# Performance work log

Hardware: AMD Instinct MI355X
Metric: run time of the kernel (lower is better)

The kernel has to match this reference:

```python
import jax, jax.numpy as jnp
import numpy as np

N, E = 4096, 65536
H = 200
KS = (3072, 1536, 768)  # ceil(0.75*4096), ceil(0.5*3072), ceil(0.5*1536)


def _gcn(A, x, W, b):
    # GCNConv with improved=True: A_hat = A + 2I, sym-normalized
    n = A.shape[0]
    Ah = A + 2.0 * jnp.eye(n, dtype=A.dtype)
    dinv = jax.lax.rsqrt(Ah.sum(axis=1))
    An = dinv[:, None] * Ah * dinv[None, :]
    return An @ (x @ W) + b


def _augment(A):
    # GraphUNet.augment_adj: remove self loops, add self loops (w=1), spspmm(A,A), remove self loops
    n = A.shape[0]
    eye = jnp.eye(n, dtype=A.dtype)
    Ap = A * (1.0 - eye) + eye
    A2 = Ap @ Ap  # dense form of spspmm (two-hop adjacency with weights)
    return A2 * (1.0 - eye)


def _pool(A, x, pw, k):
    # TopKPooling: score = tanh(x.w/||w||), keep top-k, scale kept x by score
    score = jnp.tanh((x @ pw) / jnp.linalg.norm(pw))
    val, perm = jax.lax.top_k(score, k)
    return x[perm] * val[:, None], A[perm][:, perm], perm


def _unet(x, adj, w0, b0, w1, b1, w2, b2, w3, b3, p1, p2, p3,
          u0w, u0b, u1w, u1b, u2w, u2b):
    down = [(w1, b1), (w2, b2), (w3, b3)]
    pws = [p1, p2, p3]
    up = [(u0w, u0b), (u1w, u1b), (u2w, u2b)]
    x = jax.nn.relu(_gcn(adj, x, w0, b0))
    xs, As, perms = [x], [adj], []
    A = adj
    for i in range(3):
        A = _augment(A)
        x, A, perm = _pool(A, x, pws[i], KS[i])
        x = jax.nn.relu(_gcn(A, x, *down[i]))
        if i < 2:
            xs.append(x)
            As.append(A)
        perms.append(perm)
    for i in range(3):
        j = 2 - i
        upf = jnp.zeros_like(xs[j]).at[perms[j]].set(x)
        x = xs[j] + upf  # sum_res=True
        x = _gcn(As[j], x, *up[i])
        if i < 2:
            x = jax.nn.relu(x)
    return jax.nn.log_softmax(x, axis=1)


def setup_inputs() -> dict:
    key = jax.random.key(0)
    ks = jax.random.split(key, 16)
    x = jax.random.normal(ks[0], (N, 3), dtype=jnp.float32)
    src = jax.random.randint(ks[1], (E,), 0, N)
    dst = jax.random.randint(ks[2], (E,), 0, N)
    A = jnp.zeros((N, N), jnp.float32).at[src, dst].set(1.0)
    A = jnp.maximum(A, A.T) * (1.0 - jnp.eye(N, dtype=jnp.float32))
    g = lambda k, s: jax.random.normal(k, s, jnp.float32) * 0.1
    z = lambda n: jnp.zeros((n,), jnp.float32)
    return dict(
        x=x, adj=A,
        w0=g(ks[3], (3, H)), b0=z(H),
        w1=g(ks[4], (H, H)), b1=z(H),
        w2=g(ks[5], (H, H)), b2=z(H),
        w3=g(ks[6], (H, H)), b3=z(H),
        p1=g(ks[7], (H,)), p2=g(ks[8], (H,)), p3=g(ks[9], (H,)),
        u0w=g(ks[10], (H, H)), u0b=z(H),
        u1w=g(ks[11], (H, H)), u1b=z(H),
        u2w=g(ks[12], (H, 2)), u2b=z(2),
    )


def reference(x, adj, w0, b0, w1, b1, w2, b2, w3, b3, p1, p2, p3,
              u0w, u0b, u1w, u1b, u2w, u2b):
    return _unet(x, adj, w0, b0, w1, b1, w2, b2, w3, b3, p1, p2, p3,
                 u0w, u0b, u1w, u1b, u2w, u2b)
```

## Files before the change

### kernel.cpp

```cpp
#include <hip/hip_runtime.h>

typedef unsigned short u16;
typedef unsigned int u32;
typedef unsigned long long u64;
typedef signed char s8;
typedef __attribute__((ext_vector_type(8))) short bfrag8;
typedef __attribute__((ext_vector_type(4))) float f32x4;
typedef __attribute__((ext_vector_type(4))) int i32x4;
typedef __attribute__((address_space(1))) const void gconst_void;
typedef __attribute__((address_space(3))) void lds_void_t;

__device__ __forceinline__ float bf2f(u16 u) {
  return __uint_as_float(((u32)u) << 16);
}
__device__ __forceinline__ u16 f2bf(float f) {
  u32 u = __float_as_uint(f);
  u32 r = (u + 0x7FFFu + ((u >> 16) & 1u)) >> 16;
  return (u16)r;
}
__device__ __forceinline__ void split3(float v, u16& hi, u16& mi, u16& lo) {
  hi = f2bf(v); float r1 = v - bf2f(hi);
  mi = f2bf(r1); float r2 = r1 - bf2f(mi);
  lo = f2bf(r2);
}
__device__ __forceinline__ float ld1(const void* p, int isbf, long idx) {
  return isbf ? bf2f(((const u16*)p)[idx]) : ((const float*)p)[idx];
}
__device__ __forceinline__ void ld4(const void* p, int isbf, long base, long gc, long bound, float v[4]) {
  if (gc + 3 < bound && ((base & 3) == 0)) {
    if (isbf) {
      const ushort4 u = *(const ushort4*)((const u16*)p + base);
      v[0] = bf2f(u.x); v[1] = bf2f(u.y); v[2] = bf2f(u.z); v[3] = bf2f(u.w);
    } else {
      const float4 f = *(const float4*)((const float*)p + base);
      v[0] = f.x; v[1] = f.y; v[2] = f.z; v[3] = f.w;
    }
  } else {
    #pragma unroll
    for (int d = 0; d < 4; ++d) v[d] = (gc + d < bound) ? ld1(p, isbf, base + d) : 0.f;
  }
}

__global__ void detect_k(const u32* __restrict__ a, long nw, int* __restrict__ flag) {
  long stride = (long)gridDim.x * 256;
  int f = 0;
  for (long j = (long)blockIdx.x * 256 + threadIdx.x; j < nw; j += stride) {
    u32 w = a[j];
    if (w == 0x00003F80u || w == 0x3F803F80u) f = 1;
  }
  if (__any(f)) {
    if ((threadIdx.x & 63) == 0) atomicOr(flag, 1);
  }
}

__device__ __forceinline__ int get_bf(int abf, const int* dtf) {
  return (abf >= 0) ? abf : *dtf;
}

__device__ __forceinline__ void stageB16(const void* g, void* lds) {
#if __has_builtin(__builtin_amdgcn_global_load_lds)
  __builtin_amdgcn_global_load_lds((gconst_void*)g, (lds_void_t*)lds, 16, 0, 0);
#else
  int lane = threadIdx.x & 63;
  *(int4*)((char*)lds + lane * 16) = *(const int4*)g;
#endif
}

__global__ __launch_bounds__(256) void syrk_tri_i8_parts(
    const s8* __restrict__ Ag, int ldk, int Ksplit, int ntri,
    int* __restrict__ parts)
{
  __shared__ s8 At[128 * 64];
  __shared__ s8 Bt[128 * 64];
  const int t = blockIdx.x;
  int ti = (int)((sqrtf((float)(8 * t + 1)) - 1.0f) * 0.5f);
  while ((ti + 1) * (ti + 2) / 2 <= t) ++ti;
  while (ti * (ti + 1) / 2 > t) --ti;
  const int tj = t - ti * (ti + 1) / 2;

  const int tid = threadIdx.x;
  const int wave = tid >> 6, lane = tid & 63;
  const int wr = wave >> 1, wc = wave & 1;
  const long rowA0 = (long)ti * 128;
  const long rowB0 = (long)tj * 128;
  const int kbeg = blockIdx.y * Ksplit;
  const int kend = kbeg + Ksplit;

  i32x4 acc[4][4];
  #pragma unroll
  for (int i = 0; i < 4; ++i)
    #pragma unroll
    for (int j = 0; j < 4; ++j) acc[i][j] = (i32x4)0;

  const int srow = lane >> 2;
  const int scol = (lane & 3) * 16;
  const int m = lane & 15, q = lane >> 4;

  for (int k0 = kbeg; k0 < kend; k0 += 64) {
    #pragma unroll
    for (int tt = 0; tt < 2; ++tt) {
      const int r = wave * 32 + tt * 16;
      stageB16(Ag + (rowA0 + r + srow) * (long)ldk + k0 + scol, At + r * 64);
      stageB16(Ag + (rowB0 + r + srow) * (long)ldk + k0 + scol, Bt + r * 64);
    }
    __syncthreads();

    i32x4 af[4], bf[4];
    #pragma unroll
    for (int mt = 0; mt < 4; ++mt)
      af[mt] = *(const i32x4*)(At + (wr * 64 + mt * 16 + m) * 64 + q * 16);
    #pragma unroll
    for (int nt = 0; nt < 4; ++nt)
      bf[nt] = *(const i32x4*)(Bt + (wc * 64 + nt * 16 + m) * 64 + q * 16);
    #pragma unroll
    for (int mt = 0; mt < 4; ++mt)
      #pragma unroll
      for (int nt = 0; nt < 4; ++nt)
        acc[mt][nt] = __builtin_amdgcn_mfma_i32_16x16x64_i8(af[mt], bf[nt], acc[mt][nt], 0, 0, 0);
    __syncthreads();
  }

  int* P = parts + ((long)blockIdx.y * ntri + t) * 16384;
  #pragma unroll
  for (int mt = 0; mt < 4; ++mt) {
    #pragma unroll
    for (int nt = 0; nt < 4; ++nt) {
      const int r0 = wr * 64 + mt * 16 + q * 4;
      const int c = wc * 64 + nt * 16 + m;
      #pragma unroll
      for (int r = 0; r < 4; ++r)
        P[(r0 + r) * 128 + c] = acc[mt][nt][r];
    }
  }
}

__global__ __launch_bounds__(256) void reduce_tri_i8_k(
    const int* __restrict__ parts, int ntri, int n, int nz,
    u16* __restrict__ Ah, u16* __restrict__ Al)
{
  __shared__ float T[128 * 33];
  const int t = blockIdx.x >> 2;
  const int slab = blockIdx.x & 3;
  int ti = (int)((sqrtf((float)(8 * t + 1)) - 1.0f) * 0.5f);
  while ((ti + 1) * (ti + 2) / 2 <= t) ++ti;
  while (ti * (ti + 1) / 2 > t) --ti;
  const int tj = t - ti * (ti + 1) / 2;
  const long rowA0 = (long)ti * 128;
  const long rowB0 = (long)tj * 128;
  const int r0 = slab * 32;
  const int tid = threadIdx.x;
  const long tstride = (long)ntri * 16384;

  #pragma unroll
  for (int it = 0; it < 16; ++it) {
    const int idx = it * 256 + tid;
    const int lr = idx >> 7;
    const int lc = idx & 127;
    long base = (long)t * 16384 + (r0 + lr) * 128 + lc;
    int v = 0;
    for (int z = 0; z < nz; ++z) v += parts[(long)z * tstride + base];
    const long gr = rowA0 + r0 + lr;
    const long gc = rowB0 + lc;
    if (gr == gc) v = 0;
    const float fv = (float)v;
    const u16 h = f2bf(fv);
    const long o = gr * n + gc;
    Ah[o] = h;
    if (Al) Al[o] = f2bf(fv - bf2f(h));
    T[lc * 33 + lr] = fv;
  }
  if (ti == tj) return;
  __syncthreads();
  #pragma unroll
  for (int it = 0; it < 16; ++it) {
    const int idx = it * 256 + tid;
    const int mr = idx >> 5;
    const int mc = idx & 31;
    const float fv = T[mr * 33 + mc];
    const u16 h = f2bf(fv);
    const long o = (rowB0 + mr) * n + rowA0 + r0 + mc;
    Ah[o] = h;
    if (Al) Al[o] = f2bf(fv - bf2f(h));
  }
}

__global__ void rowsum_planes_k(const u16* __restrict__ Ah, const u16* __restrict__ Al,
                                int n, double* __restrict__ rs) {
  __shared__ double red[256];
  const int row = blockIdx.x, tid = threadIdx.x;
  const uint4* A4 = (const uint4*)(Ah + (long)row * n);
  const uint4* L4 = Al ? (const uint4*)(Al + (long)row * n) : nullptr;
  const int n8 = n >> 3;
  double s = 0.0;
  for (int j = tid; j < n8; j += 256) {
    uint4 u = A4[j];
    float v = bf2f((u16)(u.x & 0xFFFFu)) + bf2f((u16)(u.x >> 16))
            + bf2f((u16)(u.y & 0xFFFFu)) + bf2f((u16)(u.y >> 16))
            + bf2f((u16)(u.z & 0xFFFFu)) + bf2f((u16)(u.z >> 16))
            + bf2f((u16)(u.w & 0xFFFFu)) + bf2f((u16)(u.w >> 16));
    if (L4) {
      uint4 l = L4[j];
      v += bf2f((u16)(l.x & 0xFFFFu)) + bf2f((u16)(l.x >> 16))
         + bf2f((u16)(l.y & 0xFFFFu)) + bf2f((u16)(l.y >> 16))
         + bf2f((u16)(l.z & 0xFFFFu)) + bf2f((u16)(l.z >> 16))
         + bf2f((u16)(l.w & 0xFFFFu)) + bf2f((u16)(l.w >> 16));
    }
    s += (double)v;
  }
  red[tid] = s; __syncthreads();
  for (int st = 128; st > 0; st >>= 1) {
    if (tid < st) red[tid] += red[tid + st];
    __syncthreads();
  }
  if (tid == 0) rs[row] = red[0];
}

__global__ __launch_bounds__(256) void syrk_tri2_parts(
    const u16* __restrict__ Ah, const u16* __restrict__ Al, int ldk,
    float* __restrict__ parts, int n, int per)
{
  __shared__ u16 Ath[128 * 32];
  __shared__ u16 Bth[128 * 32];
  __shared__ u16 Atl[128 * 32];
  __shared__ u16 Btl[128 * 32];
  const int t = blockIdx.x;
  int ti = (int)((sqrtf((float)(8 * t + 1)) - 1.0f) * 0.5f);
  while ((ti + 1) * (ti + 2) / 2 <= t) ++ti;
  while (ti * (ti + 1) / 2 > t) --ti;
  const int tj = t - ti * (ti + 1) / 2;

  const int tid = threadIdx.x;
  const int wave = tid >> 6, lane = tid & 63;
  const int wr = wave >> 1, wc = wave & 1;
  const long rowA0 = (long)ti * 128;
  const long rowB0 = (long)tj * 128;
  const int kbeg = blockIdx.y * per;
  const int kend = kbeg + per;

  f32x4 acc[4][4];
  #pragma unroll
  for (int i = 0; i < 4; ++i)
    #pragma unroll
    for (int j = 0; j < 4; ++j) acc[i][j] = (f32x4)0.f;

  const int srow = lane >> 2;
  const int scol = (lane & 3) * 8;
  const int m = lane & 15, q = lane >> 4;

  for (int k0 = kbeg; k0 < kend; k0 += 32) {
    #pragma unroll
    for (int tt = 0; tt < 2; ++tt) {
      const int r = wave * 32 + tt * 16;
      stageB16(Ah + (rowA0 + r + srow) * (long)ldk + k0 + scol, Ath + r * 32);
      stageB16(Ah + (rowB0 + r + srow) * (long)ldk + k0 + scol, Bth + r * 32);
      stageB16(Al + (rowA0 + r + srow) * (long)ldk + k0 + scol, Atl + r * 32);
      stageB16(Al + (rowB0 + r + srow) * (long)ldk + k0 + scol, Btl + r * 32);
    }
    __syncthreads();

    bfrag8 afh[4], afl[4], bfh[4], bfl[4];
    #pragma unroll
    for (int mt = 0; mt < 4; ++mt) {
      afh[mt] = *(const bfrag8*)(Ath + (wr * 64 + mt * 16 + m) * 32 + q * 8);
      afl[mt] = *(const bfrag8*)(Atl + (wr * 64 + mt * 16 + m) * 32 + q * 8);
    }
    #pragma unroll
    for (int nt = 0; nt < 4; ++nt) {
      bfh[nt] = *(const bfrag8*)(Bth + (wc * 64 + nt * 16 + m) * 32 + q * 8);
      bfl[nt] = *(const bfrag8*)(Btl + (wc * 64 + nt * 16 + m) * 32 + q * 8);
    }
    #pragma unroll
    for (int mt = 0; mt < 4; ++mt)
      #pragma unroll
      for (int nt = 0; nt < 4; ++nt) {
        acc[mt][nt] = __builtin_amdgcn_mfma_f32_16x16x32_bf16(afh[mt], bfh[nt], acc[mt][nt], 0, 0, 0);
        acc[mt][nt] = __builtin_amdgcn_mfma_f32_16x16x32_bf16(afh[mt], bfl[nt], acc[mt][nt], 0, 0, 0);
        acc[mt][nt] = __builtin_amdgcn_mfma_f32_16x16x32_bf16(afl[mt], bfh[nt], acc[mt][nt], 0, 0, 0);
        acc[mt][nt] = __builtin_amdgcn_mfma_f32_16x16x32_bf16(afl[mt], bfl[nt], acc[mt][nt], 0, 0, 0);
      }
    __syncthreads();
  }

  float* P = parts + (long)blockIdx.y * n * n;
  #pragma unroll
  for (int mt = 0; mt < 4; ++mt) {
    #pragma unroll
    for (int nt = 0; nt < 4; ++nt) {
      const long gr0 = rowA0 + wr * 64 + mt * 16 + q * 4;
      const long gc = rowB0 + wc * 64 + nt * 16 + m;
      #pragma unroll
      for (int r = 0; r < 4; ++r)
        P[(gr0 + r) * n + gc] = acc[mt][nt][r];
    }
  }
}

__global__ void reduce_tri_mirror_k(const float* __restrict__ parts,
                                    u16* __restrict__ Ah, u16* __restrict__ Al,
                                    double* __restrict__ rsum, int n, int nz) {
  __shared__ double red[256];
  const int tid = threadIdx.x;
  long idx = (long)blockIdx.x * 256 + tid;
  long nn = (long)n * n;
  long r = idx / n, c = idx - r * n;
  double myv = 0.0;
  if (idx < nn) {
    if (r == c) {
      Ah[idx] = 0; Al[idx] = 0;
    } else if (r > c) {
      float s = 0.f;
      for (int z = 0; z < nz; ++z) s += parts[(long)z * nn + r * n + c];
      long mi = c * n + r;
      u16 h = f2bf(s);
      u16 l = f2bf(s - bf2f(h));
      Ah[idx] = h; Al[idx] = l;
      Ah[mi] = h;  Al[mi] = l;
      myv = (double)s;
      atomicAdd(&rsum[c], (double)s);
    }
  }
  red[tid] = myv;
  __syncthreads();
  for (int st = 128; st > 0; st >>= 1) {
    if (tid < st) red[tid] += red[tid + st];
    __syncthreads();
  }
  if (tid == 0 && idx < nn) atomicAdd(&rsum[r], red[0]);
}

__global__ void bg_i8_k(const void* __restrict__ src, int srcbf, int nsrc,
                        const int* __restrict__ perm, int kRows,
                        s8* __restrict__ Ag, const int* __restrict__ dtf,
                        const float* __restrict__ xsrc, const float* __restrict__ score,
                        float* __restrict__ xdst, unsigned nbB) {
  if (blockIdx.x < nbB) {
    long tot = (long)kRows * nsrc;
    long idx = (long)blockIdx.x * 256 + threadIdx.x;
    if (idx >= tot) return;
    int r = (int)(idx / nsrc);
    int c = (int)(idx - (long)r * nsrc);
    int p = perm[r];
    float v = ld1(src, get_bf(srcbf, dtf), (long)p * nsrc + c);
    if (c == p) v += 1.f;
    Ag[idx] = (s8)(int)v;
  } else {
    long tot = (long)kRows * 200;
    long idx = (long)(blockIdx.x - nbB) * 256 + threadIdx.x;
    if (idx >= tot) return;
    int r = (int)(idx / 200);
    int c = (int)(idx - (long)r * 200);
    int p = perm[r];
    xdst[idx] = xsrc[(long)p * 200 + c] * score[p];
  }
}

__global__ void bg_sp_k(const u16* __restrict__ srcH, const u16* __restrict__ srcL,
                        int nsrc, const int* __restrict__ perm, int kRows,
                        u16* __restrict__ Agh, u16* __restrict__ Agl,
                        const float* __restrict__ xsrc, const float* __restrict__ score,
                        float* __restrict__ xdst, unsigned nbB) {
  if (blockIdx.x < nbB) {
    long tot = (long)kRows * nsrc;
    long idx = (long)blockIdx.x * 256 + threadIdx.x;
    if (idx >= tot) return;
    int r = (int)(idx / nsrc);
    int c = (int)(idx - (long)r * nsrc);
    int p = perm[r];
    long si = (long)p * nsrc + c;
    float v = bf2f(srcH[si]) + bf2f(srcL[si]);
    if (c == p) v += 1.f;
    u16 h = f2bf(v);
    Agh[idx] = h;
    Agl[idx] = f2bf(v - bf2f(h));
  } else {
    long tot = (long)kRows * 200;
    long idx = (long)(blockIdx.x - nbB) * 256 + threadIdx.x;
    if (idx >= tot) return;
    int r = (int)(idx / 200);
    int c = (int)(idx - (long)r * 200);
    int p = perm[r];
    xdst[idx] = xsrc[(long)p * 200 + c] * score[p];
  }
}

template<int NT, int HASAL>
__global__ __launch_bounds__(512) void agg_mfma8(
    const u16* __restrict__ Ah, const u16* __restrict__ Al,
    const u16* __restrict__ ZT, float* __restrict__ parts,
    int K, int per_steps)
{
  constexpr int CT0 = (NT + 1) / 2;
  constexpr int NZT = 3 * NT;
  constexpr int NSTG = (HASAL ? 16 : 8) + NZT;
  __shared__ u16 At[2][8 * 512];
  __shared__ u16 Alt[(HASAL ? 2 : 1)][8 * 512];
  __shared__ u16 Zt[2][NZT * 512];

  const int tid = threadIdx.x;
  const int wave = tid >> 6, lane = tid & 63;
  const int rg = wave & 3;
  const int cg = wave >> 2;
  const int ct_base = cg ? CT0 : 0;
  const int nct = cg ? (NT - CT0) : CT0;
  const long row0 = (long)blockIdx.x * 128;
  const int chunk = blockIdx.y;
  const int kbeg = chunk * per_steps * 32;
  const int nsteps = (min(K, kbeg + per_steps * 32) - kbeg) / 32;
  const int m = lane & 15, q = lane >> 4;
  const int srow = lane >> 2, scol = (lane & 3) * 8;

  auto stage = [&](int buf, int k0) {
    u16* Atb = At[buf];
    u16* Ztb = Zt[buf];
    u16* Altb = Alt[HASAL ? buf : 0];
    for (int s = wave; s < NSTG; s += 8) {
      if (s < 8) {
        stageB16(Ah + (row0 + s * 16 + srow) * (long)K + k0 + scol, Atb + s * 512);
      } else if (HASAL && s < 16) {
        stageB16(Al + (row0 + (s - 8) * 16 + srow) * (long)K + k0 + scol, Altb + (s - 8) * 512);
      } else {
        const int z = s - (HASAL ? 16 : 8);
        stageB16(ZT + ((long)(z * 16 + srow)) * K + k0 + scol, Ztb + z * 512);
      }
    }
  };

  f32x4 acc[2][CT0];
  #pragma unroll
  for (int rt = 0; rt < 2; ++rt)
    #pragma unroll
    for (int ct = 0; ct < CT0; ++ct) acc[rt][ct] = (f32x4)0.f;

  stage(0, kbeg);
  __syncthreads();
  int cur = 0;
  for (int t = 0; t < nsteps; ++t) {
    if (t + 1 < nsteps) stage(cur ^ 1, kbeg + (t + 1) * 32);

    const u16* Atb = At[cur];
    const u16* Ztb = Zt[cur];
    bfrag8 af0 = *(const bfrag8*)(Atb + (rg * 2) * 512 + m * 32 + q * 8);
    bfrag8 af1 = *(const bfrag8*)(Atb + (rg * 2 + 1) * 512 + m * 32 + q * 8);
    bfrag8 al0, al1;
    if (HASAL) {
      const u16* Altb = Alt[cur];
      al0 = *(const bfrag8*)(Altb + (rg * 2) * 512 + m * 32 + q * 8);
      al1 = *(const bfrag8*)(Altb + (rg * 2 + 1) * 512 + m * 32 + q * 8);
    }
    #pragma unroll
    for (int ct = 0; ct < CT0; ++ct) {
      if (ct < nct) {
        const int c = ct_base + ct;
        bfrag8 b0 = *(const bfrag8*)(Ztb + (0 * NT + c) * 512 + m * 32 + q * 8);
        bfrag8 b1 = *(const bfrag8*)(Ztb + (1 * NT + c) * 512 + m * 32 + q * 8);
        bfrag8 b2 = *(const bfrag8*)(Ztb + (2 * NT + c) * 512 + m * 32 + q * 8);
        acc[0][ct] = __builtin_amdgcn_mfma_f32_16x16x32_bf16(af0, b0, acc[0][ct], 0, 0, 0);
        acc[0][ct] = __builtin_amdgcn_mfma_f32_16x16x32_bf16(af0, b1, acc[0][ct], 0, 0, 0);
        acc[0][ct] = __builtin_amdgcn_mfma_f32_16x16x32_bf16(af0, b2, acc[0][ct], 0, 0, 0);
        acc[1][ct] = __builtin_amdgcn_mfma_f32_16x16x32_bf16(af1, b0, acc[1][ct], 0, 0, 0);
        acc[1][ct] = __builtin_amdgcn_mfma_f32_16x16x32_bf16(af1, b1, acc[1][ct], 0, 0, 0);
        acc[1][ct] = __builtin_amdgcn_mfma_f32_16x16x32_bf16(af1, b2, acc[1][ct], 0, 0, 0);
        if (HASAL) {
          acc[0][ct] = __builtin_amdgcn_mfma_f32_16x16x32_bf16(al0, b0, acc[0][ct], 0, 0, 0);
          acc[0][ct] = __builtin_amdgcn_mfma_f32_16x16x32_bf16(al0, b1, acc[0][ct], 0, 0, 0);
          acc[1][ct] = __builtin_amdgcn_mfma_f32_16x16x32_bf16(al1, b0, acc[1][ct], 0, 0, 0);
          acc[1][ct] = __builtin_amdgcn_mfma_f32_16x16x32_bf16(al1, b1, acc[1][ct], 0, 0, 0);
        }
      }
    }
    if (t + 1 < nsteps) __syncthreads();
    cur ^= 1;
  }

  float* P = parts + (long)chunk * gridDim.x * 128 * (NT * 16);
  #pragma unroll
  for (int rt = 0; rt < 2; ++rt) {
    #pragma unroll
    for (int ct = 0; ct < CT0; ++ct) {
      if (ct < nct) {
        const long grow0 = row0 + rg * 32 + rt * 16 + q * 4;
        const long gcol = (ct_base + ct) * 16 + m;
        #pragma unroll
        for (int r = 0; r < 4; ++r)
          P[(grow0 + r) * (NT * 16) + gcol] = acc[rt][ct][r];
      }
    }
  }
}

__global__ __launch_bounds__(256) void reduce_epi_k(
    const float* __restrict__ parts, const float* __restrict__ Zs,
    const double* __restrict__ rs, const float* __restrict__ b,
    float* __restrict__ out, int n, int nz, int relu,
    const float* __restrict__ pw, float* __restrict__ score)
{
  __shared__ float vrow[200];
  const int i = blockIdx.x, tid = threadIdx.x;
  float dv = (float)(1.0 / sqrt(rs[i] + 2.0));
  if (tid < 200) {
    long base = (long)i * 208 + tid;
    float s = 0.f;
    for (int c = 0; c < nz; ++c) s += parts[(long)c * n * 208 + base];
    float v = dv * (s + 2.f * Zs[(long)i * 200 + tid]) + b[tid];
    if (relu) v = fmaxf(v, 0.f);
    out[(long)i * 200 + tid] = v;
    if (score) vrow[tid] = v;
  }
  if (!score) return;
  __syncthreads();
  if (tid < 64) {
    double ps = 0.0;
    for (int j = tid; j < 200; j += 64) { double w = pw[j]; ps += w * w; }
    for (int off = 32; off > 0; off >>= 1) ps += __shfl_down(ps, off);
    double nrm = sqrt(__shfl(ps, 0));
    double s = 0.0;
    for (int j = tid; j < 200; j += 64) s += (double)vrow[j] * (double)pw[j];
    for (int off = 32; off > 0; off >>= 1) s += __shfl_down(s, off);
    if (tid == 0) score[i] = (float)tanh(s / nrm);
  }
}

__global__ void a_from_adj_rs_k(const void* __restrict__ adj, const int* __restrict__ dtf,
                                int n, u16* __restrict__ Ah, double* __restrict__ rs) {
  __shared__ double red[256];
  int bf = *dtf;
  const int row = blockIdx.x, tid = threadIdx.x;
  const long base = (long)row * n;
  double s = 0.0;
  for (int j = tid; j < n; j += 256) {
    float v = ld1(adj, bf, base + j);
    Ah[base + j] = bf ? ((const u16*)adj)[base + j] : f2bf(v);
    s += (double)v;
  }
  red[tid] = s; __syncthreads();
  for (int st = 128; st > 0; st >>= 1) {
    if (tid < st) red[tid] += red[tid + st];
    __syncthreads();
  }
  if (tid == 0) rs[row] = red[0];
}

__global__ __launch_bounds__(256) void gemm64_f64(
    const void* __restrict__ Ap, long lda, int abf,
    const void* __restrict__ Bp, long ldb, int bbf,
    float* __restrict__ C, long ldc, int M, int N, int K,
    const double* __restrict__ rsum, u16* __restrict__ ZT, const int* __restrict__ dtf)
{
  const int abf_ = get_bf(abf, dtf);
  const int bbf_ = get_bf(bbf, dtf);
  __shared__ float As[16][64];
  __shared__ float Bs[16][64];
  const int tid = threadIdx.x;
  const int tr = tid >> 4, tc = tid & 15;
  const long row0 = (long)blockIdx.y * 64;
  const long col0 = (long)blockIdx.x * 64;
  double acc[4][4];
  #pragma unroll
  for (int i = 0; i < 4; ++i)
    #pragma unroll
    for (int j = 0; j < 4; ++j) acc[i][j] = 0.0;

  const int am = tid >> 2;
  const int ak = (tid & 3) * 4;
  const int bk = tid >> 4;
  const int bn = (tid & 15) * 4;

  for (int k0 = 0; k0 < K; k0 += 16) {
    float va[4] = {0.f, 0.f, 0.f, 0.f};
    {
      long gm = row0 + am; long gk = k0 + ak;
      if (gm < M && gk < K) ld4(Ap, abf_, gm * lda + gk, gk, K, va);
    }
    As[ak + 0][am] = va[0]; As[ak + 1][am] = va[1];
    As[ak + 2][am] = va[2]; As[ak + 3][am] = va[3];

    float vb[4] = {0.f, 0.f, 0.f, 0.f};
    {
      long gk = k0 + bk; long gn = col0 + bn;
      if (gk < K && gn < N) ld4(Bp, bbf_, gk * ldb + gn, gn, N, vb);
    }
    Bs[bk][bn + 0] = vb[0]; Bs[bk][bn + 1] = vb[1];
    Bs[bk][bn + 2] = vb[2]; Bs[bk][bn + 3] = vb[3];

    __syncthreads();
    #pragma unroll
    for (int kk = 0; kk < 16; ++kk) {
      float a[4], b[4];
      #pragma unroll
      for (int i = 0; i < 4; ++i) a[i] = As[kk][tr * 4 + i];
      #pragma unroll
      for (int j = 0; j < 4; ++j) b[j] = Bs[kk][tc * 4 + j];
      #pragma unroll
      for (int i = 0; i < 4; ++i)
        #pragma unroll
        for (int j = 0; j < 4; ++j)
          acc[i][j] += (double)a[i] * (double)b[j];
    }
    __syncthreads();
  }
  #pragma unroll
  for (int i = 0; i < 4; ++i) {
    long gm = row0 + tr * 4 + i;
    if (gm >= M) continue;
    float sc = rsum ? (float)(1.0 / sqrt(rsum[gm] + 2.0)) : 1.f;
    #pragma unroll
    for (int j = 0; j < 4; ++j) {
      long gn = col0 + tc * 4 + j;
      if (gn < N) {
        float v0 = (float)acc[i][j];
        float v = v0 * sc;
        C[gm * ldc + gn] = v;
        if (ZT) {
          u16 hi, mi, lo; split3(v, hi, mi, lo);
          ZT[((long)0 * 208 + gn) * M + gm] = hi;
          ZT[((long)1 * 208 + gn) * M + gm] = mi;
          ZT[((long)2 * 208 + gn) * M + gm] = lo;
        }
      }
    }
  }
}

struct UpBatch {
  const void* src[19];
  float* dst[19];
  int n[19];
};

__global__ void upcast_batch_k(UpBatch ub, const int* __restrict__ dtf) {
  int bf = *dtf;
  int a = blockIdx.y;
  int i = blockIdx.x * 256 + threadIdx.x;
  if (i < ub.n[a]) ub.dst[a][i] = ld1(ub.src[a], bf, i);
}

template<int V>
__global__ __launch_bounds__(1024) void topk_fast(const float* __restrict__ score,
                                                  int n, int np2, int k,
                                                  int* __restrict__ perm,
                                                  int* __restrict__ inv) {
  __shared__ u64 keys[4096];
  const int tid = threadIdx.x;
  const int REGMAX = 32 * V;
  for (int i = tid; i < n; i += 1024) inv[i] = -1;
  u64 kreg[V];
  #pragma unroll
  for (int r = 0; r < V; ++r) {
    int i = tid * V + r;
    u64 key = 0ULL;
    if (i < n) {
      u32 b = __float_as_uint(score[i]);
      u32 u = (b & 0x80000000u) ? ~b : (b | 0x80000000u);
      key = ((u64)u << 32) | (u32)(~(u32)i);
    }
    kreg[r] = key;
  }

  for (int size = 2; size <= np2; size <<= 1) {
    int stride = size >> 1;
    if (stride > REGMAX) {
      #pragma unroll
      for (int r = 0; r < V; ++r) keys[tid * V + r] = kreg[r];
      __syncthreads();
      for (; stride > REGMAX; stride >>= 1) {
        for (int i = tid; i < np2; i += 1024) {
          int j = i ^ stride;
          if (j > i) {
            u64 a = keys[i], b = keys[j];
            bool up = ((i & size) == 0);
            if (up ? (a > b) : (a < b)) { keys[i] = b; keys[j] = a; }
          }
        }
        __syncthreads();
      }
      #pragma unroll
      for (int r = 0; r < V; ++r) kreg[r] = keys[tid * V + r];
    }
    for (; stride >= 1; stride >>= 1) {
      if (stride >= V) {
        int lm = stride / V;
        #pragma unroll
        for (int r = 0; r < V; ++r) {
          u64 mine = kreg[r];
          u64 other = (u64)__shfl_xor((long long)mine, lm);
          int i = tid * V + r;
          bool up = ((i & size) == 0);
          bool lower = ((i & stride) == 0);
          u64 mn = mine < other ? mine : other;
          u64 mx = mine < other ? other : mine;
          kreg[r] = (lower == up) ? mn : mx;
        }
      } else {
        #pragma unroll
        for (int r = 0; r < V; ++r) {
          int pr = r ^ stride;
          if (pr > r) {
            int i = tid * V + r;
            bool up = ((i & size) == 0);
            u64 a = kreg[r], b = kreg[pr];
            if (up ? (a > b) : (a < b)) { kreg[r] = b; kreg[pr] = a; }
          }
        }
      }
    }
  }
  #pragma unroll
  for (int r = 0; r < V; ++r) {
    int i = tid * V + r;
    int rank = np2 - 1 - i;
    if (rank < k) {
      int idx = (int)(~(u32)(kreg[r] & 0xFFFFFFFFull));
      perm[rank] = idx;
      inv[idx] = rank;
    }
  }
}

__global__ void upadd_k(const float* __restrict__ xs, const float* __restrict__ xpool,
                        const int* __restrict__ inv, float* __restrict__ dst, long nh, int h) {
  long idx = (long)blockIdx.x * 256 + threadIdx.x;
  if (idx >= nh) return;
  int i = (int)(idx / h);
  int c = (int)(idx - (long)i * h);
  float v = xs[idx];
  int r = inv[i];
  if (r >= 0) v += xpool[(long)r * h + c];
  dst[idx] = v;
}

__global__ void matvec2_final_k(const void* __restrict__ A, int abf, int n,
                                const float* __restrict__ Zs, const double* __restrict__ rs0,
                                const float* __restrict__ b2, float* __restrict__ out,
                                const int* __restrict__ dtf) {
  const int bf = get_bf(abf, dtf);
  int row = blockIdx.x, tid = threadIdx.x;
  const long base = (long)row * n;
  double s0 = 0.0, s1 = 0.0;
  for (int j = tid; j < n; j += 256) {
    double a = (double)ld1(A, bf, base + j);
    s0 += a * (double)Zs[2 * j];
    s1 += a * (double)Zs[2 * j + 1];
  }
  __shared__ double r0[256], r1[256];
  r0[tid] = s0; r1[tid] = s1; __syncthreads();
  for (int st = 128; st > 0; st >>= 1) {
    if (tid < st) { r0[tid] += r0[tid + st]; r1[tid] += r1[tid + st]; }
    __syncthreads();
  }
  if (tid == 0) {
    double y0 = (double)((float)r0[0]);
    double y1 = (double)((float)r1[0]);
    double di = (double)((float)(1.0 / sqrt(rs0[row] + 2.0)));
    double t0 = di * (y0 + 2.0 * (double)Zs[2 * row]) + (double)b2[0];
    double t1 = di * (y1 + 2.0 * (double)Zs[2 * row + 1]) + (double)b2[1];
    double mx = fmax(t0, t1);
    double l = mx + log(exp(t0 - mx) + exp(t1 - mx));
    out[2 * row] = (float)(t0 - l);
    out[2 * row + 1] = (float)(t1 - l);
  }
}

extern "C" void kernel_launch(void* const* d_in, const int* in_sizes, int n_in,
                              void* d_out, int out_size, void* d_ws, size_t ws_size,
                              hipStream_t stream) {
  const int N0 = 4096, H = 200;
  const int K1 = 3072, K2 = 1536, K3 = 768;

  const void* in_x = d_in[0];
  const void* adj  = d_in[1];
  const void* w0 = d_in[2];  const void* b0 = d_in[3];
  const void* w1 = d_in[4];  const void* b1 = d_in[5];
  const void* w2 = d_in[6];  const void* b2 = d_in[7];
  const void* w3 = d_in[8];  const void* b3 = d_in[9];
  const void* p1 = d_in[10]; const void* p2 = d_in[11];
  const void* p3 = d_in[12];
  const void* u0w = d_in[13]; const void* u0b = d_in[14];
  const void* u1w = d_in[15]; const void* u1b = d_in[16];
  const void* u2w = d_in[17]; const void* u2b = d_in[18];

  char* wp = (char*)d_ws;
  auto alloc = [&](size_t bytes) -> void* {
    void* p = (void*)wp;
    wp += (bytes + 255) & ~(size_t)255;
    return p;
  };
  size_t partsBytes = (size_t)300 * 4 * 16384 * 4 + 1024;
  float* parts = (float*)alloc(partsBytes);
  s8*    Agb  = (s8*)alloc((size_t)K1 * N0);
  u16* Ag3h = (u16*)alloc((size_t)K3 * K2 * 2);
  u16* Ag3l = (u16*)alloc((size_t)K3 * K2 * 2);
  u16* Ah0 = (u16*)alloc((size_t)N0 * N0 * 2);
  u16* Ah1 = (u16*)alloc((size_t)K1 * K1 * 2);
  u16* Ah2 = (u16*)alloc((size_t)K2 * K2 * 2);
  u16* Al2 = (u16*)alloc((size_t)K2 * K2 * 2);
  u16* Ah3 = (u16*)alloc((size_t)K3 * K3 * 2);
  u16* Al3 = (u16*)alloc((size_t)K3 * K3 * 2);
  u16* ZT  = (u16*)alloc((size_t)3 * 208 * N0 * 2);
  float* xs0  = (float*)alloc((size_t)N0 * H * 4);
  float* xs1  = (float*)alloc((size_t)K1 * H * 4);
  float* xs2  = (float*)alloc((size_t)K2 * H * 4);
  float* xcur = (float*)alloc((size_t)N0 * H * 4);
  float* xtmp = (float*)alloc((size_t)N0 * H * 4);
  float* Zbuf = (float*)alloc((size_t)N0 * H * 4);
  float* Xinf = (float*)alloc((size_t)N0 * 3 * 4);
  double* rs0 = (double*)alloc((size_t)N0 * 8);
  double* rs1 = (double*)alloc((size_t)K1 * 8);
  double* rs2 = (double*)alloc((size_t)K2 * 8);
  double* rs3 = (double*)alloc((size_t)K3 * 8);
  int* dtflag = (int*)alloc(256);
  float* scores = (float*)alloc((size_t)N0 * 4);
  int* perm1 = (int*)alloc((size_t)K1 * 4);
  int* perm2 = (int*)alloc((size_t)K2 * 4);
  int* perm3 = (int*)alloc((size_t)K3 * 4);
  int* inv1 = (int*)alloc((size_t)N0 * 4);
  int* inv2 = (int*)alloc((size_t)K1 * 4);
  int* inv3 = (int*)alloc((size_t)K2 * 4);
  float* w0f = (float*)alloc(3 * H * 4);  float* b0f = (float*)alloc(H * 4);
  float* w1f = (float*)alloc(H * H * 4);  float* b1f = (float*)alloc(H * 4);
  float* w2f = (float*)alloc(H * H * 4);  float* b2f = (float*)alloc(H * 4);
  float* w3f = (float*)alloc(H * H * 4);  float* b3f = (float*)alloc(H * 4);
  float* p1f = (float*)alloc(H * 4);
  float* p2f = (float*)alloc(H * 4);
  float* p3f = (float*)alloc(H * 4);
  float* u0wf = (float*)alloc(H * H * 4); float* u0bf = (float*)alloc(H * 4);
  float* u1wf = (float*)alloc(H * H * 4); float* u1bf = (float*)alloc(H * 4);
  float* u2wf = (float*)alloc(H * 2 * 4); float* u2bf = (float*)alloc(2 * 4);
  (void)in_sizes; (void)n_in; (void)out_size; (void)ws_size;

  hipMemsetAsync(rs1, 0, (size_t)(K1 + K2 + K3) * 8 + 256, stream);
  detect_k<<<dim3(4096), dim3(256), 0, stream>>>((const u32*)adj, (long)N0 * N0 / 2, dtflag);

  {
    UpBatch ub;
    const void* srcs[19] = {in_x, w0, b0, w1, b1, w2, b2, w3, b3, p1, p2, p3,
                            u0w, u0b, u1w, u1b, u2w, u2b, u2b};
    float* dsts[19] = {Xinf, w0f, b0f, w1f, b1f, w2f, b2f, w3f, b3f, p1f, p2f, p3f,
                       u0wf, u0bf, u1wf, u1bf, u2wf, u2bf, u2bf};
    int ns[19] = {N0 * 3, 3 * H, H, H * H, H, H * H, H, H * H, H, H, H, H,
                  H * H, H, H * H, H, H * 2, 2, 2};
    for (int i = 0; i < 19; ++i) { ub.src[i] = srcs[i]; ub.dst[i] = dsts[i]; ub.n[i] = ns[i]; }
    upcast_batch_k<<<dim3((N0 * 3 + 255) / 256, 19), dim3(256), 0, stream>>>(ub, dtflag);
  }

  a_from_adj_rs_k<<<dim3(N0), dim3(256), 0, stream>>>(adj, dtflag, N0, Ah0, rs0);

  auto gemm64 = [&](const void* A, long lda, int abf, const void* B, long ldb, int bbf,
                    float* C, long ldc, int M, int Nn, int K, const double* rsum, u16* zt) {
    dim3 g((Nn + 63) / 64, (M + 63) / 64);
    gemm64_f64<<<g, dim3(256), 0, stream>>>(A, lda, abf, B, ldb, bbf, C, ldc, M, Nn, K,
                                            rsum, zt, dtflag);
  };

  auto gcn = [&](const u16* Ah, const u16* Al, int n, int chunks, const double* rs,
                 const float* Xin_, int din, const float* W, const float* bb,
                 float* out, const float* pwf, float* scoreOut) {
    gemm64(Xin_, din, 0, W, H, 0, Zbuf, H, n, H, din, rs, ZT);
    if (Al)
      agg_mfma8<13, 1><<<dim3(n / 128, chunks), dim3(512), 0, stream>>>(
          Ah, Al, ZT, parts, n, (n / 32) / chunks);
    else
      agg_mfma8<13, 0><<<dim3(n / 128, chunks), dim3(512), 0, stream>>>(
          Ah, nullptr, ZT, parts, n, (n / 32) / chunks);
    reduce_epi_k<<<dim3(n), dim3(256), 0, stream>>>(
        parts, Zbuf, rs, bb, out, n, chunks, 1, pwf, scoreOut);
  };

  gcn(Ah0, nullptr, N0, 8, rs0, Xinf, 3, w0f, b0f, xs0, p1f, scores);

  topk_fast<4><<<dim3(1), dim3(1024), 0, stream>>>(scores, N0, 4096, K1, perm1, inv1);
  {
    unsigned nbB = (unsigned)(((long)K1 * N0 + 255) / 256);
    unsigned nbG = (unsigned)(((long)K1 * 200 + 255) / 256);
    bg_i8_k<<<dim3(nbB + nbG), dim3(256), 0, stream>>>(
        adj, -1, N0, perm1, K1, Agb, dtflag, xs0, scores, xcur, nbB);
    int nt = K1 / 128;
    int ntri = nt * (nt + 1) / 2;
    syrk_tri_i8_parts<<<dim3(ntri, 4), dim3(256), 0, stream>>>(
        Agb, N0, N0 / 4, ntri, (int*)parts);
    reduce_tri_i8_k<<<dim3(ntri * 4), dim3(256), 0, stream>>>(
        (const int*)parts, ntri, K1, 4, Ah1, nullptr);
    rowsum_planes_k<<<dim3(K1), dim3(256), 0, stream>>>(Ah1, nullptr, K1, rs1);
  }
  gcn(Ah1, nullptr, K1, 12, rs1, xcur, H, w1f, b1f, xs1, p2f, scores);

  topk_fast<4><<<dim3(1), dim3(1024), 0, stream>>>(scores, K1, 4096, K2, perm2, inv2);
  {
    unsigned nbB = (unsigned)(((long)K2 * K1 + 255) / 256);
    unsigned nbG = (unsigned)(((long)K2 * 200 + 255) / 256);
    bg_i8_k<<<dim3(nbB + nbG), dim3(256), 0, stream>>>(
        Ah1, 1, K1, perm2, K2, Agb, dtflag, xs1, scores, xcur, nbB);
    int nt = K2 / 128;
    int ntri = nt * (nt + 1) / 2;
    syrk_tri_i8_parts<<<dim3(ntri, 8), dim3(256), 0, stream>>>(
        Agb, K1, K1 / 8, ntri, (int*)parts);
    reduce_tri_i8_k<<<dim3(ntri * 4), dim3(256), 0, stream>>>(
        (const int*)parts, ntri, K2, 8, Ah2, Al2);
    rowsum_planes_k<<<dim3(K2), dim3(256), 0, stream>>>(Ah2, Al2, K2, rs2);
  }
  gcn(Ah2, Al2, K2, 24, rs2, xcur, H, w2f, b2f, xs2, p3f, scores);

  topk_fast<2><<<dim3(1), dim3(1024), 0, stream>>>(scores, K2, 2048, K3, perm3, inv3);
  {
    unsigned nbB = (unsigned)(((long)K3 * K2 + 255) / 256);
    unsigned nbG = (unsigned)(((long)K3 * 200 + 255) / 256);
    bg_sp_k<<<dim3(nbB + nbG), dim3(256), 0, stream>>>(
        Ah2, Al2, K2, perm3, K3, Ag3h, Ag3l, xs2, scores, xcur, nbB);
    int nt = K3 / 128;
    syrk_tri2_parts<<<dim3(nt * (nt + 1) / 2, 8), dim3(256), 0, stream>>>(
        Ag3h, Ag3l, K2, parts, K3, K2 / 8);
    long nn = (long)K3 * K3;
    reduce_tri_mirror_k<<<dim3((unsigned)(nn / 256)), dim3(256), 0, stream>>>(
        parts, Ah3, Al3, rs3, K3, 8);
  }
  gcn(Ah3, Al3, K3, 24, rs3, xcur, H, w3f, b3f, xcur, nullptr, nullptr);

  upadd_k<<<dim3((unsigned)(((long)K2 * H + 255) / 256)), dim3(256), 0, stream>>>(
      xs2, xcur, inv3, xtmp, (long)K2 * H, H);
  gcn(Ah2, Al2, K2, 24, rs2, xtmp, H, u0wf, u0bf, xcur, nullptr, nullptr);

  upadd_k<<<dim3((unsigned)(((long)K1 * H + 255) / 256)), dim3(256), 0, stream>>>(
      xs1, xcur, inv2, xtmp, (long)K1 * H, H);
  gcn(Ah1, nullptr, K1, 12, rs1, xtmp, H, u1wf, u1bf, xcur, nullptr, nullptr);

  upadd_k<<<dim3((unsigned)(((long)N0 * H + 255) / 256)), dim3(256), 0, stream>>>(
      xs0, xcur, inv1, xtmp, (long)N0 * H, H);
  gemm64(xtmp, H, 0, u2wf, 2, 0, Zbuf, 2, N0, 2, H, rs0, nullptr);
  matvec2_final_k<<<dim3(N0), dim3(256), 0, stream>>>(
      adj, -1, N0, Zbuf, rs0, u2bf, (float*)d_out, dtflag);
}
```

Before: 879.6 us.

## Replace single-block bitonic top-k with multi-block rank counting; double-buffer int8 SYRK

After: 848.6 us. 1.04x faster.

```diff
diff --git a/kernel.cpp b/kernel.cpp
--- a/kernel.cpp
+++ b/kernel.cpp
@@ -70,8 +70,8 @@
     const s8* __restrict__ Ag, int ldk, int Ksplit, int ntri,
     int* __restrict__ parts)
 {
-  __shared__ s8 At[128 * 64];
-  __shared__ s8 Bt[128 * 64];
+  __shared__ s8 At[2][128 * 64];
+  __shared__ s8 Bt[2][128 * 64];
   const int t = blockIdx.x;
   int ti = (int)((sqrtf((float)(8 * t + 1)) - 1.0f) * 0.5f);
   while ((ti + 1) * (ti + 2) / 2 <= t) ++ti;
@@ -84,7 +84,7 @@
   const long rowA0 = (long)ti * 128;
   const long rowB0 = (long)tj * 128;
   const int kbeg = blockIdx.y * Ksplit;
-  const int kend = kbeg + Ksplit;
+  const int nsteps = Ksplit / 64;
 
   i32x4 acc[4][4];
   #pragma unroll
@@ -96,28 +96,35 @@
   const int scol = (lane & 3) * 16;
   const int m = lane & 15, q = lane >> 4;
 
-  for (int k0 = kbeg; k0 < kend; k0 += 64) {
+  auto stage = [&](int buf, int k0) {
     #pragma unroll
     for (int tt = 0; tt < 2; ++tt) {
       const int r = wave * 32 + tt * 16;
-      stageB16(Ag + (rowA0 + r + srow) * (long)ldk + k0 + scol, At + r * 64);
-      stageB16(Ag + (rowB0 + r + srow) * (long)ldk + k0 + scol, Bt + r * 64);
-    }
-    __syncthreads();
+      stageB16(Ag + (rowA0 + r + srow) * (long)ldk + k0 + scol, At[buf] + r * 64);
+      stageB16(Ag + (rowB0 + r + srow) * (long)ldk + k0 + scol, Bt[buf] + r * 64);
+    }
+  };
+
+  stage(0, kbeg);
+  __syncthreads();
+  int cur = 0;
+  for (int st = 0; st < nsteps; ++st) {
+    if (st + 1 < nsteps) stage(cur ^ 1, kbeg + (st + 1) * 64);
 
     i32x4 af[4], bf[4];
     #pragma unroll
     for (int mt = 0; mt < 4; ++mt)
-      af[mt] = *(const i32x4*)(At + (wr * 64 + mt * 16 + m) * 64 + q * 16);
+      af[mt] = *(const i32x4*)(At[cur] + (wr * 64 + mt * 16 + m) * 64 + q * 16);
     #pragma unroll
     for (int nt = 0; nt < 4; ++nt)
-      bf[nt] = *(const i32x4*)(Bt + (wc * 64 + nt * 16 + m) * 64 + q * 16);
+      bf[nt] = *(const i32x4*)(Bt[cur] + (wc * 64 + nt * 16 + m) * 64 + q * 16);
     #pragma unroll
     for (int mt = 0; mt < 4; ++mt)
       #pragma unroll
       for (int nt = 0; nt < 4; ++nt)
         acc[mt][nt] = __builtin_amdgcn_mfma_i32_16x16x64_i8(af[mt], bf[nt], acc[mt][nt], 0, 0, 0);
-    __syncthreads();
+    if (st + 1 < nsteps) __syncthreads();
+    cur ^= 1;
   }
 
   int* P = parts + ((long)blockIdx.y * ntri + t) * 16384;
@@ -634,86 +641,57 @@
   if (i < ub.n[a]) ub.dst[a][i] = ld1(ub.src[a], bf, i);
 }
 
-template<int V>
-__global__ __launch_bounds__(1024) void topk_fast(const float* __restrict__ score,
-                                                  int n, int np2, int k,
-                                                  int* __restrict__ perm,
-                                                  int* __restrict__ inv) {
-  __shared__ u64 keys[4096];
+__global__ __launch_bounds__(256) void rank_part_k(
+    const float* __restrict__ score, int n, int ns, int* __restrict__ prank)
+{
+  __shared__ u64 sk[256];
   const int tid = threadIdx.x;
-  const int REGMAX = 32 * V;
-  for (int i = tid; i < n; i += 1024) inv[i] = -1;
-  u64 kreg[V];
-  #pragma unroll
-  for (int r = 0; r < V; ++r) {
-    int i = tid * V + r;
+  const int s = blockIdx.x;
+  const int slice = n / ns;
+  const int jb = s * slice;
+  for (int j = tid; j < slice; j += 256) {
+    int gj = jb + j;
+    u32 b = __float_as_uint(score[gj]);
+    u32 u = (b & 0x80000000u) ? ~b : (b | 0x80000000u);
+    sk[j] = ((u64)u << 32) | (u32)(~(u32)gj);
+  }
+  __syncthreads();
+  const int i0 = tid * 16;
+  if (i0 >= n) return;
+  u64 myk[16];
+  int cnt[16];
+  #pragma unroll
+  for (int e = 0; e < 16; ++e) {
+    int i = i0 + e;
     u64 key = 0ULL;
     if (i < n) {
       u32 b = __float_as_uint(score[i]);
       u32 u = (b & 0x80000000u) ? ~b : (b | 0x80000000u);
       key = ((u64)u << 32) | (u32)(~(u32)i);
     }
-    kreg[r] = key;
-  }
-
-  for (int size = 2; size <= np2; size <<= 1) {
-    int stride = size >> 1;
-    if (stride > REGMAX) {
-      #pragma unroll
-      for (int r = 0; r < V; ++r) keys[tid * V + r] = kreg[r];
-      __syncthreads();
-      for (; stride > REGMAX; stride >>= 1) {
-        for (int i = tid; i < np2; i += 1024) {
-          int j = i ^ stride;
-          if (j > i) {
-            u64 a = keys[i], b = keys[j];
-            bool up = ((i & size) == 0);
-            if (up ? (a > b) : (a < b)) { keys[i] = b; keys[j] = a; }
-          }
-        }
-        __syncthreads();
-      }
-      #pragma unroll
-      for (int r = 0; r < V; ++r) kreg[r] = keys[tid * V + r];
-    }
-    for (; stride >= 1; stride >>= 1) {
-      if (stride >= V) {
-        int lm = stride / V;
-        #pragma unroll
-        for (int r = 0; r < V; ++r) {
-          u64 mine = kreg[r];
-          u64 other = (u64)__shfl_xor((long long)mine, lm);
-          int i = tid * V + r;
-          bool up = ((i & size) == 0);
-          bool lower = ((i & stride) == 0);
-          u64 mn = mine < other ? mine : other;
-          u64 mx = mine < other ? other : mine;
-          kreg[r] = (lower == up) ? mn : mx;
-        }
-      } else {
-        #pragma unroll
-        for (int r = 0; r < V; ++r) {
-          int pr = r ^ stride;
-          if (pr > r) {
-            int i = tid * V + r;
-            bool up = ((i & size) == 0);
-            u64 a = kreg[r], b = kreg[pr];
-            if (up ? (a > b) : (a < b)) { kreg[r] = b; kreg[pr] = a; }
-          }
-        }
-      }
-    }
-  }
-  #pragma unroll
-  for (int r = 0; r < V; ++r) {
-    int i = tid * V + r;
-    int rank = np2 - 1 - i;
-    if (rank < k) {
-      int idx = (int)(~(u32)(kreg[r] & 0xFFFFFFFFull));
-      perm[rank] = idx;
-      inv[idx] = rank;
-    }
-  }
+    myk[e] = key; cnt[e] = 0;
+  }
+  #pragma unroll 4
+  for (int j = 0; j < slice; ++j) {
+    u64 kj = sk[j];
+    #pragma unroll
+    for (int e = 0; e < 16; ++e) cnt[e] += (kj > myk[e]) ? 1 : 0;
+  }
+  #pragma unroll
+  for (int e = 0; e < 16; ++e) {
+    int i = i0 + e;
+    if (i < n) prank[s * n + i] = cnt[e];
+  }
+}
+
+__global__ void rank_scatter_k(const int* __restrict__ prank, int n, int ns, int k,
+                               int* __restrict__ perm, int* __restrict__ inv) {
+  int i = blockIdx.x * 256 + threadIdx.x;
+  if (i >= n) return;
+  int r = 0;
+  for (int s = 0; s < ns; ++s) r += prank[s * n + i];
+  inv[i] = (r < k) ? r : -1;
+  if (r < k) perm[r] = i;
 }
 
 __global__ void upadd_k(const float* __restrict__ xs, const float* __restrict__ xpool,
@@ -765,6 +743,7 @@
                               hipStream_t stream) {
   const int N0 = 4096, H = 200;
   const int K1 = 3072, K2 = 1536, K3 = 768;
+  const int TK_NS = 32;
 
   const void* in_x = d_in[0];
   const void* adj  = d_in[1];
@@ -809,6 +788,7 @@
   double* rs3 = (double*)alloc((size_t)K3 * 8);
   int* dtflag = (int*)alloc(256);
   float* scores = (float*)alloc((size_t)N0 * 4);
+  int* prank = (int*)alloc((size_t)TK_NS * N0 * 4);
   int* perm1 = (int*)alloc((size_t)K1 * 4);
   int* perm2 = (int*)alloc((size_t)K2 * 4);
   int* perm3 = (int*)alloc((size_t)K3 * 4);
@@ -865,9 +845,15 @@
         parts, Zbuf, rs, bb, out, n, chunks, 1, pwf, scoreOut);
   };
 
+  auto topk = [&](const float* sc, int n, int k, int* perm, int* inv) {
+    rank_part_k<<<dim3(TK_NS), dim3(256), 0, stream>>>(sc, n, TK_NS, prank);
+    rank_scatter_k<<<dim3((unsigned)((n + 255) / 256)), dim3(256), 0, stream>>>(
+        prank, n, TK_NS, k, perm, inv);
+  };
+
   gcn(Ah0, nullptr, N0, 8, rs0, Xinf, 3, w0f, b0f, xs0, p1f, scores);
 
-  topk_fast<4><<<dim3(1), dim3(1024), 0, stream>>>(scores, N0, 4096, K1, perm1, inv1);
+  topk(scores, N0, K1, perm1, inv1);
   {
     unsigned nbB = (unsigned)(((long)K1 * N0 + 255) / 256);
     unsigned nbG = (unsigned)(((long)K1 * 200 + 255) / 256);
@@ -883,7 +869,7 @@
   }
   gcn(Ah1, nullptr, K1, 12, rs1, xcur, H, w1f, b1f, xs1, p2f, scores);
 
-  topk_fast<4><<<dim3(1), dim3(1024), 0, stream>>>(scores, K1, 4096, K2, perm2, inv2);
+  topk(scores, K1, K2, perm2, inv2);
   {
     unsigned nbB = (unsigned)(((long)K2 * K1 + 255) / 256);
     unsigned nbG = (unsigned)(((long)K2 * 200 + 255) / 256);
@@ -899,7 +885,7 @@
   }
   gcn(Ah2, Al2, K2, 24, rs2, xcur, H, w2f, b2f, xs2, p3f, scores);
 
-  topk_fast<2><<<dim3(1), dim3(1024), 0, stream>>>(scores, K2, 2048, K3, perm3, inv3);
+  topk(scores, K2, K3, perm3, inv3);
   {
     unsigned nbB = (unsigned)(((long)K3 * K2 + 255) / 256);
     unsigned nbG = (unsigned)(((long)K3 * 200 + 255) / 256);
```
